# Performance work log

Hardware: AMD Instinct MI355X
Metric: run time of the kernel (lower is better)

Reference implementation:

```python
import jax, jax.numpy as jnp
import numpy as np

B, N, K = 2, 65536, 16
D_OUT, D_FEAT = 64, 64
EPS = 1e-6


def setup_inputs() -> dict:
    key = jax.random.key(0)
    ks = jax.random.split(key, 8)
    coords = jax.random.normal(ks[0], (B, N, 3), dtype=jnp.float32)
    features = jax.random.normal(ks[1], (B, D_FEAT, N, 1), dtype=jnp.float32)
    knn_points = jax.random.randint(ks[2], (B, N, K), 0, N)
    knn_dist = jax.random.uniform(ks[3], (B, N, K), dtype=jnp.float32)
    # SharedMLP params: 1x1 Conv2d(10 -> D_OUT) + BatchNorm2d(D_OUT)
    W = jax.random.normal(ks[4], (D_OUT, 10), dtype=jnp.float32) * 0.1
    b = jnp.zeros((D_OUT,), dtype=jnp.float32)
    gamma = jnp.ones((D_OUT,), dtype=jnp.float32)
    beta = jnp.zeros((D_OUT,), dtype=jnp.float32)
    return {"coords": coords, "features": features, "knn_points": knn_points,
            "knn_dist": knn_dist, "W": W, "b": b, "gamma": gamma, "beta": beta}


def reference(coords, features, knn_points, knn_dist, W, b, gamma, beta):
    Bd, Nd, Kd = knn_points.shape
    # gather neighbor xyz: neighbors[b,n,k,:] = coords[b, knn_points[b,n,k], :]
    nb = jax.vmap(lambda c, i: c[i])(coords, knn_points)          # [B,N,K,3]
    nb = jnp.transpose(nb, (0, 3, 1, 2))                          # [B,3,N,K]
    center = jnp.broadcast_to(
        jnp.transpose(coords, (0, 2, 1))[..., None], (Bd, 3, Nd, Kd))  # [B,3,N,K]
    # 10-channel spatial encoding: xyz, neighbor xyz, relative xyz, distance
    sp = jnp.concatenate([center, nb, center - nb, knn_dist[:, None]], axis=1)  # [B,10,N,K]
    # 1x1 conv
    x = jnp.einsum('oc,bcnk->bonk', W, sp) + b[None, :, None, None]  # [B,D_OUT,N,K]
    # BatchNorm2d in training mode: batch statistics over (B,N,K) per channel
    mean = x.mean(axis=(0, 2, 3))
    var = x.var(axis=(0, 2, 3))
    x = (x - mean[None, :, None, None]) * jax.lax.rsqrt(var + EPS)[None, :, None, None]
    x = x * gamma[None, :, None, None] + beta[None, :, None, None]
    x = jax.nn.relu(x)
    feat = jnp.broadcast_to(features, (Bd, features.shape[1], Nd, Kd))
    return jnp.concatenate([x, feat], axis=1)  # [B, D_OUT+D_FEAT, N, K]
```

## Files before the change

kernel.cpp:

```cpp
#include <hip/hip_runtime.h>
#include <hip/hip_bf16.h>

#define N_PTS 65536
#define BATCH 2
#define KNN   16
#define NBLK_V2 2048
#define NBLK_V1 512

typedef float float4n __attribute__((ext_vector_type(4)));

__device__ __forceinline__ int tri(int i, int j) {
    return i * 7 - (i * (i - 1)) / 2 + (j - i);
}

__global__ __launch_bounds__(256) void k_stats4(const float* __restrict__ coords,
                                                const int* __restrict__ knn,
                                                const float* __restrict__ dist,
                                                float* __restrict__ partials) {
    int gid = blockIdx.x * 256 + threadIdx.x;
    int q  = gid & 3;
    int pp = gid >> 2;
    int b  = pp >> 16;
    const float* cp = coords + (size_t)pp * 3;
    float cx = cp[0], cy = cp[1], cz = cp[2];
    const float* cb = coords + (size_t)b * (N_PTS * 3);

    int4   ia = *(const int4*)  (knn  + ((size_t)pp << 4) + (q << 2));
    float4 da = *(const float4*)(dist + ((size_t)pp << 4) + (q << 2));
    int   idx[4] = {ia.x, ia.y, ia.z, ia.w};
    float dd[4]  = {da.x, da.y, da.z, da.w};

    float s[35];
#pragma unroll
    for (int i = 0; i < 35; i++) s[i] = 0.f;

#pragma unroll
    for (int k = 0; k < 4; k++) {
        const float* qq = cb + (size_t)idx[k] * 3;
        float v[7];
        v[0] = cx; v[1] = cy; v[2] = cz;
        v[3] = qq[0]; v[4] = qq[1]; v[5] = qq[2];
        v[6] = dd[k];
        int t = 7;
#pragma unroll
        for (int i = 0; i < 7; i++) {
            s[i] += v[i];
#pragma unroll
            for (int j = i; j < 7; j++) { s[t] += v[i] * v[j]; t++; }
        }
    }

    __shared__ float red[4][35];
    int lane = threadIdx.x & 63;
    int wid  = threadIdx.x >> 6;
#pragma unroll
    for (int i = 0; i < 35; i++) {
        float v = s[i];
#pragma unroll
        for (int off = 32; off; off >>= 1) v += __shfl_xor(v, off);
        if (lane == 0) red[wid][i] = v;
    }
    __syncthreads();
    if (threadIdx.x < 35) {
        int i = threadIdx.x;
        partials[i * NBLK_V2 + blockIdx.x] =
            (red[0][i] + red[1][i]) + (red[2][i] + red[3][i]);
    }
}

__global__ __launch_bounds__(256) void k_prep256(const float* __restrict__ W,
                                                 const float* __restrict__ bias,
                                                 const float* __restrict__ gamma,
                                                 const float* __restrict__ beta,
                                                 const float* __restrict__ partials,
                                                 float* __restrict__ w8) {
    __shared__ float red[4][35];
    __shared__ float sst[35];
    int t = threadIdx.x;
    float acc[35];
    const float* p0 = partials + t * 8;
#pragma unroll
    for (int i = 0; i < 35; i++) {
        const float* p = p0 + i * NBLK_V2;
        float4 a = *(const float4*)p;
        float4 c = *(const float4*)(p + 4);
        acc[i] = ((a.x + a.y) + (a.z + a.w)) + ((c.x + c.y) + (c.z + c.w));
    }
    int lane = t & 63, wid = t >> 6;
#pragma unroll
    for (int i = 0; i < 35; i++) {
        float v = acc[i];
#pragma unroll
        for (int off = 32; off; off >>= 1) v += __shfl_xor(v, off);
        if (lane == 0) red[wid][i] = v;
    }
    __syncthreads();
    if (t < 35) sst[t] = (red[0][t] + red[1][t]) + (red[2][t] + red[3][t]);
    __syncthreads();

    if (t >= 64) return;
    int o = t;
    const float invM = 1.0f / (float)((size_t)BATCH * N_PTS * KNN);
    float m[7];
#pragma unroll
    for (int j = 0; j < 7; j++) m[j] = sst[j] * invM;
    const float* Wo = W + o * 10;
    float wv[7];
    wv[0] = Wo[0] + Wo[6]; wv[1] = Wo[1] + Wo[7]; wv[2] = Wo[2] + Wo[8];
    wv[3] = Wo[3] - Wo[6]; wv[4] = Wo[4] - Wo[7]; wv[5] = Wo[5] - Wo[8];
    wv[6] = Wo[9];
    float mean = bias[o];
#pragma unroll
    for (int j = 0; j < 7; j++) mean += wv[j] * m[j];
    float var = 0.f;
#pragma unroll
    for (int i = 0; i < 7; i++) {
#pragma unroll
        for (int j = 0; j < 7; j++) {
            int a = i < j ? i : j, c = i < j ? j : i;
            float cov = sst[7 + tri(a, c)] * invM - m[i] * m[j];
            var += wv[i] * wv[j] * cov;
        }
    }
    float s = gamma[o] * rsqrtf(var + 1e-6f);
    float sh = beta[o] - mean * s;
#pragma unroll
    for (int j = 0; j < 7; j++) w8[o * 8 + j] = s * wv[j];
    w8[o * 8 + 7] = s * bias[o] + sh;
}

__global__ __launch_bounds__(256) void k_stats_fb(const float* __restrict__ coords,
                                                  const int* __restrict__ knn,
                                                  const float* __restrict__ dist,
                                                  float* __restrict__ stats_atomic,
                                                  float* __restrict__ partials,
                                                  int use_part) {
    int gid = blockIdx.x * 256 + threadIdx.x;
    int b = gid >> 16;
    const float* cp = coords + (size_t)gid * 3;
    float cx = cp[0], cy = cp[1], cz = cp[2];
    const float* cb = coords + (size_t)b * (N_PTS * 3);
    const int* ip = knn + ((size_t)gid << 4);
    const float* dp = dist + ((size_t)gid << 4);

    float s[35];
#pragma unroll
    for (int i = 0; i < 35; i++) s[i] = 0.f;
    for (int k = 0; k < KNN; k++) {
        int idx = ip[k];
        const float* q = cb + (size_t)idx * 3;
        float v[7];
        v[0] = cx; v[1] = cy; v[2] = cz;
        v[3] = q[0]; v[4] = q[1]; v[5] = q[2];
        v[6] = dp[k];
        int t = 7;
#pragma unroll
        for (int i = 0; i < 7; i++) {
            s[i] += v[i];
#pragma unroll
            for (int j = i; j < 7; j++) { s[t] += v[i] * v[j]; t++; }
        }
    }
    __shared__ float red[4][35];
    int lane = threadIdx.x & 63;
    int wid  = threadIdx.x >> 6;
#pragma unroll
    for (int i = 0; i < 35; i++) {
        float v = s[i];
#pragma unroll
        for (int off = 32; off; off >>= 1) v += __shfl_xor(v, off);
        if (lane == 0) red[wid][i] = v;
    }
    __syncthreads();
    if (threadIdx.x < 35) {
        int i = threadIdx.x;
        float v = (red[0][i] + red[1][i]) + (red[2][i] + red[3][i]);
        if (use_part) partials[i * NBLK_V1 + blockIdx.x] = v;
        else          atomicAdd(&stats_atomic[i], v);
    }
}

__global__ __launch_bounds__(64) void k_prep_fb(const float* __restrict__ W,
                                                const float* __restrict__ bias,
                                                const float* __restrict__ gamma,
                                                const float* __restrict__ beta,
                                                const float* __restrict__ stats_atomic,
                                                const float* __restrict__ partials,
                                                int use_part,
                                                float* __restrict__ w8) {
    __shared__ float sst[35];
    int t = threadIdx.x;
    if (t < 35) {
        if (use_part) {
            const float* p = partials + t * NBLK_V1;
            float a0 = 0.f, a1 = 0.f, a2 = 0.f, a3 = 0.f;
            for (int j = 0; j < NBLK_V1; j += 4) {
                a0 += p[j]; a1 += p[j + 1]; a2 += p[j + 2]; a3 += p[j + 3];
            }
            sst[t] = (a0 + a1) + (a2 + a3);
        } else {
            sst[t] = stats_atomic[t];
        }
    }
    __syncthreads();
    int o = t;
    const float invM = 1.0f / (float)((size_t)BATCH * N_PTS * KNN);
    float m[7];
#pragma unroll
    for (int j = 0; j < 7; j++) m[j] = sst[j] * invM;
    const float* Wo = W + o * 10;
    float wv[7];
    wv[0] = Wo[0] + Wo[6]; wv[1] = Wo[1] + Wo[7]; wv[2] = Wo[2] + Wo[8];
    wv[3] = Wo[3] - Wo[6]; wv[4] = Wo[4] - Wo[7]; wv[5] = Wo[5] - Wo[8];
    wv[6] = Wo[9];
    float mean = bias[o];
#pragma unroll
    for (int j = 0; j < 7; j++) mean += wv[j] * m[j];
    float var = 0.f;
#pragma unroll
    for (int i = 0; i < 7; i++) {
#pragma unroll
        for (int j = 0; j < 7; j++) {
            int a = i < j ? i : j, c = i < j ? j : i;
            float cov = sst[7 + tri(a, c)] * invM - m[i] * m[j];
            var += wv[i] * wv[j] * cov;
        }
    }
    float s = gamma[o] * rsqrtf(var + 1e-6f);
    float sh = beta[o] - mean * s;
#pragma unroll
    for (int j = 0; j < 7; j++) w8[o * 8 + j] = s * wv[j];
    w8[o * 8 + 7] = s * bias[o] + sh;
}

__global__ __launch_bounds__(256) void k_x(const float* __restrict__ coords,
                                           const int* __restrict__ knn,
                                           const float* __restrict__ dist,
                                           const float* __restrict__ w8g,
                                           float* __restrict__ out) {
    __shared__ float w8[512];
    for (int i = threadIdx.x; i < 512; i += 256) w8[i] = w8g[i];
    __syncthreads();

    int gid = blockIdx.x * 256 + threadIdx.x;
    int q  = gid & 3;
    int pp = gid >> 2;
    int b = pp >> 16;
    int n = pp & 0xFFFF;

    const float* cp = coords + (size_t)pp * 3;
    float cx = cp[0], cy = cp[1], cz = cp[2];
    const float* cb = coords + (size_t)b * (N_PTS * 3);

    int4   ia = *(const int4*)  (knn  + ((size_t)pp << 4) + (q << 2));
    float4 da = *(const float4*)(dist + ((size_t)pp << 4) + (q << 2));
    int   idx[4] = {ia.x, ia.y, ia.z, ia.w};
    float dd[4]  = {da.x, da.y, da.z, da.w};
    float nx[4], ny[4], nz[4];
#pragma unroll
    for (int k = 0; k < 4; k++) {
        const float* qq = cb + (size_t)idx[k] * 3;
        nx[k] = qq[0]; ny[k] = qq[1]; nz[k] = qq[2];
    }

    size_t base = ((size_t)b * 128) * (N_PTS * KNN) + (size_t)n * KNN + (q << 2);
#pragma unroll 4
    for (int c = 0; c < 64; c++) {
        float4 wa = *reinterpret_cast<const float4*>(&w8[c << 3]);
        float4 wb = *reinterpret_cast<const float4*>(&w8[(c << 3) + 4]);
        float s0 = fmaf(cx, wa.x, fmaf(cy, wa.y, fmaf(cz, wa.z, wb.w)));
        float x[4];
#pragma unroll
        for (int k = 0; k < 4; k++) {
            float v = fmaf(dd[k], wb.z, fmaf(nz[k], wb.y, fmaf(ny[k], wb.x, fmaf(nx[k], wa.w, s0))));
            x[k] = fmaxf(v, 0.f);
        }
        float4n v0 = {x[0], x[1], x[2], x[3]};
        __builtin_nontemporal_store(v0,
            reinterpret_cast<float4n*>(out + base + (size_t)c * (N_PTS * KNN)));
    }
}

__global__ __launch_bounds__(256) void k_feat(const float* __restrict__ feat,
                                              float* __restrict__ out) {
    int gid = blockIdx.x * 256 + threadIdx.x;
    int q4 = gid & 3;
    int r  = gid >> 2;
    float v = feat[r];
    int b = r >> 22;
    int f = (r >> 16) & 63;
    int n = r & 0xFFFF;
    size_t base = (((size_t)b * 128 + 64 + f) * N_PTS + n) * KNN + (q4 << 2);
    float4n vv = {v, v, v, v};
    __builtin_nontemporal_store(vv, reinterpret_cast<float4n*>(out + base));
}

extern "C" void kernel_launch(void* const* d_in, const int* in_sizes, int n_in,
                              void* d_out, int out_size, void* d_ws, size_t ws_size,
                              hipStream_t stream) {
    const float* coords   = (const float*)d_in[0];
    const float* features = (const float*)d_in[1];
    const int*   knn      = (const int*)d_in[2];
    const float* dist     = (const float*)d_in[3];
    const float* W        = (const float*)d_in[4];
    const float* bias     = (const float*)d_in[5];
    const float* gamma    = (const float*)d_in[6];
    const float* beta     = (const float*)d_in[7];
    float* out            = (float*)d_out;

    float* stats    = (float*)d_ws;
    float* w8       = stats + 64;
    float* partials = w8 + 512;
    size_t need2 = (64 + 512 + 35 * NBLK_V2) * sizeof(float);
    size_t need1 = (64 + 512 + 35 * NBLK_V1) * sizeof(float);

    if (ws_size >= need2) {
        k_stats4<<<NBLK_V2, 256, 0, stream>>>(coords, knn, dist, partials);
        k_prep256<<<1, 256, 0, stream>>>(W, bias, gamma, beta, partials, w8);
    } else {
        int use_part = (ws_size >= need1) ? 1 : 0;
        if (!use_part)
            (void)hipMemsetAsync(d_ws, 0, 64 * sizeof(float), stream);
        k_stats_fb<<<NBLK_V1, 256, 0, stream>>>(coords, knn, dist, stats, partials, use_part);
        k_prep_fb<<<1, 64, 0, stream>>>(W, bias, gamma, beta, stats, partials, use_part, w8);
    }
    k_x<<<2048, 256, 0, stream>>>(coords, knn, dist, w8, out);
    k_feat<<<131072, 256, 0, stream>>>(features, out);
}
```

Baseline: 243.8 us.

## Fuse feature broadcast into stats kernel and factor moment accumulation

The feature-broadcast writes are folded into the statistics kernel as extra blocks, so the stats reduction runs alongside the large feature store instead of as a separate short launch. The per-thread second-moment accumulation is also restructured: center coordinates are constant per thread, so center products are computed once and multiplied by per-point neighbor sums rather than recomputed for each neighbor. This removes one kernel launch and cuts stats arithmetic, at the cost of a heterogeneous grid whose stats blocks may finish unevenly and delay the prep kernel.

After: 232.1 us. 1.05x faster.

```diff
diff --git a/kernel.cpp b/kernel.cpp
--- a/kernel.cpp
+++ b/kernel.cpp
@@ -4,7 +4,7 @@
 #define N_PTS 65536
 #define BATCH 2
 #define KNN   16
-#define NBLK_V2 2048
+#define NBLK_S2 2048
 #define NBLK_V1 512
 
 typedef float float4n __attribute__((ext_vector_type(4)));
@@ -13,58 +13,77 @@
     return i * 7 - (i * (i - 1)) / 2 + (j - i);
 }
 
-__global__ __launch_bounds__(256) void k_stats4(const float* __restrict__ coords,
-                                                const int* __restrict__ knn,
-                                                const float* __restrict__ dist,
-                                                float* __restrict__ partials) {
-    int gid = blockIdx.x * 256 + threadIdx.x;
-    int q  = gid & 3;
-    int pp = gid >> 2;
-    int b  = pp >> 16;
-    const float* cp = coords + (size_t)pp * 3;
-    float cx = cp[0], cy = cp[1], cz = cp[2];
-    const float* cb = coords + (size_t)b * (N_PTS * 3);
-
-    int4   ia = *(const int4*)  (knn  + ((size_t)pp << 4) + (q << 2));
-    float4 da = *(const float4*)(dist + ((size_t)pp << 4) + (q << 2));
-    int   idx[4] = {ia.x, ia.y, ia.z, ia.w};
-    float dd[4]  = {da.x, da.y, da.z, da.w};
-
-    float s[35];
-#pragma unroll
-    for (int i = 0; i < 35; i++) s[i] = 0.f;
-
-#pragma unroll
-    for (int k = 0; k < 4; k++) {
-        const float* qq = cb + (size_t)idx[k] * 3;
-        float v[7];
-        v[0] = cx; v[1] = cy; v[2] = cz;
-        v[3] = qq[0]; v[4] = qq[1]; v[5] = qq[2];
-        v[6] = dd[k];
-        int t = 7;
-#pragma unroll
-        for (int i = 0; i < 7; i++) {
-            s[i] += v[i];
-#pragma unroll
-            for (int j = i; j < 7; j++) { s[t] += v[i] * v[j]; t++; }
-        }
-    }
-
-    __shared__ float red[4][35];
-    int lane = threadIdx.x & 63;
-    int wid  = threadIdx.x >> 6;
-#pragma unroll
-    for (int i = 0; i < 35; i++) {
-        float v = s[i];
-#pragma unroll
-        for (int off = 32; off; off >>= 1) v += __shfl_xor(v, off);
-        if (lane == 0) red[wid][i] = v;
-    }
-    __syncthreads();
-    if (threadIdx.x < 35) {
-        int i = threadIdx.x;
-        partials[i * NBLK_V2 + blockIdx.x] =
-            (red[0][i] + red[1][i]) + (red[2][i] + red[3][i]);
+__global__ __launch_bounds__(256) void k_featstats(const float* __restrict__ feat,
+                                                   float* __restrict__ out,
+                                                   const float* __restrict__ coords,
+                                                   const int* __restrict__ knn,
+                                                   const float* __restrict__ dist,
+                                                   float* __restrict__ partials) {
+    int bid = blockIdx.x;
+    if (bid < NBLK_S2) {
+        int gid = bid * 256 + threadIdx.x;
+        int q  = gid & 3;
+        int pp = gid >> 2;
+        int b  = pp >> 16;
+        const float* cp = coords + (size_t)pp * 3;
+        float cx = cp[0], cy = cp[1], cz = cp[2];
+        const float* cb = coords + (size_t)b * (N_PTS * 3);
+
+        int4   ia = *(const int4*)  (knn  + ((size_t)pp << 4) + (q << 2));
+        float4 da = *(const float4*)(dist + ((size_t)pp << 4) + (q << 2));
+        int   idx[4] = {ia.x, ia.y, ia.z, ia.w};
+        float dd[4]  = {da.x, da.y, da.z, da.w};
+
+        float Gx = 0.f, Gy = 0.f, Gz = 0.f, D1 = 0.f, D2 = 0.f;
+        float Sxx = 0.f, Sxy = 0.f, Sxz = 0.f, Syy = 0.f, Syz = 0.f, Szz = 0.f;
+        float NDx = 0.f, NDy = 0.f, NDz = 0.f;
+#pragma unroll
+        for (int k = 0; k < 4; k++) {
+            const float* qq = cb + (size_t)idx[k] * 3;
+            float nx = qq[0], ny = qq[1], nz = qq[2], d = dd[k];
+            Gx += nx; Gy += ny; Gz += nz; D1 += d; D2 += d * d;
+            Sxx += nx * nx; Sxy += nx * ny; Sxz += nx * nz;
+            Syy += ny * ny; Syz += ny * nz; Szz += nz * nz;
+            NDx += nx * d; NDy += ny * d; NDz += nz * d;
+        }
+
+        __shared__ float red[4][35];
+        int lane = threadIdx.x & 63, wid = threadIdx.x >> 6;
+        int slot = 0;
+#define RED1(expr) { float v_ = (expr); \
+        v_ += __shfl_xor(v_, 32); v_ += __shfl_xor(v_, 16); \
+        v_ += __shfl_xor(v_, 8);  v_ += __shfl_xor(v_, 4);  \
+        v_ += __shfl_xor(v_, 2);  v_ += __shfl_xor(v_, 1);  \
+        if (lane == 0) red[wid][slot] = v_; slot++; }
+        RED1(4.f*cx) RED1(4.f*cy) RED1(4.f*cz) RED1(Gx) RED1(Gy) RED1(Gz) RED1(D1)
+        RED1(4.f*cx*cx) RED1(4.f*cx*cy) RED1(4.f*cx*cz)
+        RED1(cx*Gx) RED1(cx*Gy) RED1(cx*Gz) RED1(cx*D1)
+        RED1(4.f*cy*cy) RED1(4.f*cy*cz)
+        RED1(cy*Gx) RED1(cy*Gy) RED1(cy*Gz) RED1(cy*D1)
+        RED1(4.f*cz*cz)
+        RED1(cz*Gx) RED1(cz*Gy) RED1(cz*Gz) RED1(cz*D1)
+        RED1(Sxx) RED1(Sxy) RED1(Sxz) RED1(NDx)
+        RED1(Syy) RED1(Syz) RED1(NDy)
+        RED1(Szz) RED1(NDz)
+        RED1(D2)
+#undef RED1
+        __syncthreads();
+        if (threadIdx.x < 35) {
+            int i = threadIdx.x;
+            partials[i * NBLK_S2 + bid] =
+                (red[0][i] + red[1][i]) + (red[2][i] + red[3][i]);
+        }
+    } else {
+        int gid = (bid - NBLK_S2) * 256 + threadIdx.x;
+        int q4 = gid & 3;
+        int r  = gid >> 2;
+        float v = feat[r];
+        int b = r >> 22;
+        int f = (r >> 16) & 63;
+        int n = r & 0xFFFF;
+        size_t base = (((size_t)b * 128 + 64 + f) * N_PTS + n) * KNN + (q4 << 2);
+        float4n vv = {v, v, v, v};
+        __builtin_nontemporal_store(vv, reinterpret_cast<float4n*>(out + base));
     }
 }
 
@@ -81,7 +100,7 @@
     const float* p0 = partials + t * 8;
 #pragma unroll
     for (int i = 0; i < 35; i++) {
-        const float* p = p0 + i * NBLK_V2;
+        const float* p = p0 + i * NBLK_S2;
         float4 a = *(const float4*)p;
         float4 c = *(const float4*)(p + 4);
         acc[i] = ((a.x + a.y) + (a.z + a.w)) + ((c.x + c.y) + (c.z + c.w));
@@ -233,54 +252,6 @@
     w8[o * 8 + 7] = s * bias[o] + sh;
 }
 
-__global__ __launch_bounds__(256) void k_x(const float* __restrict__ coords,
-                                           const int* __restrict__ knn,
-                                           const float* __restrict__ dist,
-                                           const float* __restrict__ w8g,
-                                           float* __restrict__ out) {
-    __shared__ float w8[512];
-    for (int i = threadIdx.x; i < 512; i += 256) w8[i] = w8g[i];
-    __syncthreads();
-
-    int gid = blockIdx.x * 256 + threadIdx.x;
-    int q  = gid & 3;
-    int pp = gid >> 2;
-    int b = pp >> 16;
-    int n = pp & 0xFFFF;
-
-    const float* cp = coords + (size_t)pp * 3;
-    float cx = cp[0], cy = cp[1], cz = cp[2];
-    const float* cb = coords + (size_t)b * (N_PTS * 3);
-
-    int4   ia = *(const int4*)  (knn  + ((size_t)pp << 4) + (q << 2));
-    float4 da = *(const float4*)(dist + ((size_t)pp << 4) + (q << 2));
-    int   idx[4] = {ia.x, ia.y, ia.z, ia.w};
-    float dd[4]  = {da.x, da.y, da.z, da.w};
-    float nx[4], ny[4], nz[4];
-#pragma unroll
-    for (int k = 0; k < 4; k++) {
-        const float* qq = cb + (size_t)idx[k] * 3;
-        nx[k] = qq[0]; ny[k] = qq[1]; nz[k] = qq[2];
-    }
-
-    size_t base = ((size_t)b * 128) * (N_PTS * KNN) + (size_t)n * KNN + (q << 2);
-#pragma unroll 4
-    for (int c = 0; c < 64; c++) {
-        float4 wa = *reinterpret_cast<const float4*>(&w8[c << 3]);
-        float4 wb = *reinterpret_cast<const float4*>(&w8[(c << 3) + 4]);
-        float s0 = fmaf(cx, wa.x, fmaf(cy, wa.y, fmaf(cz, wa.z, wb.w)));
-        float x[4];
-#pragma unroll
-        for (int k = 0; k < 4; k++) {
-            float v = fmaf(dd[k], wb.z, fmaf(nz[k], wb.y, fmaf(ny[k], wb.x, fmaf(nx[k], wa.w, s0))));
-            x[k] = fmaxf(v, 0.f);
-        }
-        float4n v0 = {x[0], x[1], x[2], x[3]};
-        __builtin_nontemporal_store(v0,
-            reinterpret_cast<float4n*>(out + base + (size_t)c * (N_PTS * KNN)));
-    }
-}
-
 __global__ __launch_bounds__(256) void k_feat(const float* __restrict__ feat,
                                               float* __restrict__ out) {
     int gid = blockIdx.x * 256 + threadIdx.x;
@@ -295,6 +266,54 @@
     __builtin_nontemporal_store(vv, reinterpret_cast<float4n*>(out + base));
 }
 
+__global__ __launch_bounds__(256) void k_x(const float* __restrict__ coords,
+                                           const int* __restrict__ knn,
+                                           const float* __restrict__ dist,
+                                           const float* __restrict__ w8g,
+                                           float* __restrict__ out) {
+    __shared__ float w8[512];
+    for (int i = threadIdx.x; i < 512; i += 256) w8[i] = w8g[i];
+    __syncthreads();
+
+    int gid = blockIdx.x * 256 + threadIdx.x;
+    int q  = gid & 3;
+    int pp = gid >> 2;
+    int b = pp >> 16;
+    int n = pp & 0xFFFF;
+
+    const float* cp = coords + (size_t)pp * 3;
+    float cx = cp[0], cy = cp[1], cz = cp[2];
+    const float* cb = coords + (size_t)b * (N_PTS * 3);
+
+    int4   ia = *(const int4*)  (knn  + ((size_t)pp << 4) + (q << 2));
+    float4 da = *(const float4*)(dist + ((size_t)pp << 4) + (q << 2));
+    int   idx[4] = {ia.x, ia.y, ia.z, ia.w};
+    float dd[4]  = {da.x, da.y, da.z, da.w};
+    float nx[4], ny[4], nz[4];
+#pragma unroll
+    for (int k = 0; k < 4; k++) {
+        const float* qq = cb + (size_t)idx[k] * 3;
+        nx[k] = qq[0]; ny[k] = qq[1]; nz[k] = qq[2];
+    }
+
+    size_t base = ((size_t)b * 128) * (N_PTS * KNN) + (size_t)n * KNN + (q << 2);
+#pragma unroll 4
+    for (int c = 0; c < 64; c++) {
+        float4 wa = *reinterpret_cast<const float4*>(&w8[c << 3]);
+        float4 wb = *reinterpret_cast<const float4*>(&w8[(c << 3) + 4]);
+        float s0 = fmaf(cx, wa.x, fmaf(cy, wa.y, fmaf(cz, wa.z, wb.w)));
+        float x[4];
+#pragma unroll
+        for (int k = 0; k < 4; k++) {
+            float v = fmaf(dd[k], wb.z, fmaf(nz[k], wb.y, fmaf(ny[k], wb.x, fmaf(nx[k], wa.w, s0))));
+            x[k] = fmaxf(v, 0.f);
+        }
+        float4n v0 = {x[0], x[1], x[2], x[3]};
+        __builtin_nontemporal_store(v0,
+            reinterpret_cast<float4n*>(out + base + (size_t)c * (N_PTS * KNN)));
+    }
+}
+
 extern "C" void kernel_launch(void* const* d_in, const int* in_sizes, int n_in,
                               void* d_out, int out_size, void* d_ws, size_t ws_size,
                               hipStream_t stream) {
@@ -311,11 +330,12 @@
     float* stats    = (float*)d_ws;
     float* w8       = stats + 64;
     float* partials = w8 + 512;
-    size_t need2 = (64 + 512 + 35 * NBLK_V2) * sizeof(float);
+    size_t need2 = (64 + 512 + 35 * NBLK_S2) * sizeof(float);
     size_t need1 = (64 + 512 + 35 * NBLK_V1) * sizeof(float);
 
     if (ws_size >= need2) {
-        k_stats4<<<NBLK_V2, 256, 0, stream>>>(coords, knn, dist, partials);
+        k_featstats<<<NBLK_S2 + 131072, 256, 0, stream>>>(features, out, coords, knn, dist,
+                                                          partials);
         k_prep256<<<1, 256, 0, stream>>>(W, bias, gamma, beta, partials, w8);
     } else {
         int use_part = (ws_size >= need1) ? 1 : 0;
@@ -323,7 +343,7 @@
             (void)hipMemsetAsync(d_ws, 0, 64 * sizeof(float), stream);
         k_stats_fb<<<NBLK_V1, 256, 0, stream>>>(coords, knn, dist, stats, partials, use_part);
         k_prep_fb<<<1, 64, 0, stream>>>(W, bias, gamma, beta, stats, partials, use_part, w8);
+        k_feat<<<131072, 256, 0, stream>>>(features, out);
     }
     k_x<<<2048, 256, 0, stream>>>(coords, knn, dist, w8, out);
-    k_feat<<<131072, 256, 0, stream>>>(features, out);
-}
+}
```
